# Performance work log

Hardware: AMD Instinct MI355X
Metric: run time of the kernel (lower is better)

## Reference

```python
import jax, jax.numpy as jnp
import numpy as np

EPS = 1e-6


def _att_vector(x, W, b, sharp2, th2, is_last):
    """AttentionVector on a 2D payoff slice.
    x: (N, a, m). W: (1, 2), b: (1,). Returns (N, a)."""
    # compare_param: pair (x[n,j,k], x[n,i,k]) -> Linear(2,1) -> sigmoid -> mean over k
    # Linear on the concat pair is w00*x[n,j,k] + w01*x[n,i,k] + b, so we fuse it.
    lin = W[0, 0] * x[:, None, :, :] + W[0, 1] * x[:, :, None, :] + b[0]  # (N,a,a,m)
    c = jnp.mean(jax.nn.sigmoid(lin), axis=3)  # (N,a,a)
    # max_normalize over dim 2
    c = c / (jnp.max(c, axis=2, keepdims=True) + EPS)
    # compute_player_mask
    m = jnp.mean(c, axis=2)  # (N,a)
    m = jax.nn.relu(m * sharp2[0] + th2[0])
    m = jax.nn.softmax(m, axis=1)
    if not is_last:
        m = m / (jnp.max(m, axis=1, keepdims=True) + EPS)
    return m


def setup_inputs() -> dict:
    key = jax.random.key(0)
    ks = jax.random.split(key, 16)
    N, a1, a2, f = 128, 64, 64, 2
    inp = {
        "x": jax.random.normal(ks[0], (N, f, a1, a2), dtype=jnp.float32),
        "fc_W": jax.random.normal(ks[1], (2, 2), dtype=jnp.float32) * 0.5,
        "fc_b": jax.random.normal(ks[2], (2,), dtype=jnp.float32) * 0.1,
        "p1_W": jax.random.normal(ks[3], (1, 2), dtype=jnp.float32) * 0.5,
        "p1_b": jax.random.normal(ks[4], (1,), dtype=jnp.float32) * 0.1,
        "p1_sharp": jnp.ones((1,), dtype=jnp.float32),
        "p1_th": jnp.zeros((1,), dtype=jnp.float32),
        "p2_W": jax.random.normal(ks[5], (1, 2), dtype=jnp.float32) * 0.5,
        "p2_b": jax.random.normal(ks[6], (1,), dtype=jnp.float32) * 0.1,
        "p2_sharp": jnp.ones((1,), dtype=jnp.float32),
        "p2_th": jnp.zeros((1,), dtype=jnp.float32),
        "out_W": jax.random.normal(ks[7], (1, 2), dtype=jnp.float32) * 0.5,
        "out_b": jax.random.normal(ks[8], (1,), dtype=jnp.float32) * 0.1,
        "out_sharp": jnp.ones((1,), dtype=jnp.float32),
        "out_th": jnp.zeros((1,), dtype=jnp.float32),
    }
    return inp


def reference(x, fc_W, fc_b, p1_W, p1_b, p1_sharp, p1_th,
              p2_W, p2_b, p2_sharp, p2_th,
              out_W, out_b, out_sharp, out_th):
    # x: (N, f=2, a1, a2) -> (N, a1, a2, f)
    h = jnp.transpose(x, (0, 2, 3, 1))
    # is_fc_first: Linear(2, 2) + ReLU on last dim
    h = jax.nn.relu(h @ fc_W.T + fc_b)  # (N,a1,a2,2)
    # one AttentionModule (module_layers=1, not simult)
    vec1 = _att_vector(h[..., 0], p1_W, p1_b, p1_sharp, p1_th, is_last=False)  # (N,a1)
    h = h * vec1[:, :, None, None]
    pl2 = jnp.transpose(h[..., 1], (0, 2, 1))  # (N,a2,a1)
    vec2 = _att_vector(pl2, p2_W, p2_b, p2_sharp, p2_th, is_last=False)  # (N,a2)
    h = h * vec2[:, None, :, None]
    # with_last: final AttentionVector (is_last=True) on player-1 channel
    out = _att_vector(h[..., 0], out_W, out_b, out_sharp, out_th, is_last=True)  # (N,a1)
    return out
```

## Files before the change

kernel.cpp:

```cpp
#include <hip/hip_runtime.h>


constexpr int A   = 64;
constexpr int PAD = 65;
constexpr float L2E  = 1.4426950408889634f;
constexpr float EPSF = 1e-6f;

__device__ __forceinline__ float bcast(float v, int srcLane) {
    return __int_as_float(__builtin_amdgcn_readlane(__float_as_int(v), srcLane));
}
__device__ __forceinline__ float rcpf(float v) { return __builtin_amdgcn_rcpf(v); }
__device__ __forceinline__ float ex2(float v)  { return __builtin_amdgcn_exp2f(v); }

__device__ __forceinline__ void att2q(const float* __restrict__ prow,
                                      const float* __restrict__ qL,
                                      int row0, int lane,
                                      float* __restrict__ mbuf,
                                      float* __restrict__ mg)
{
    const float qreg0 = qL[row0 * PAD + lane];
    const float qreg1 = qL[(row0 + 1) * PAD + lane];
    float acc0 = 0.f, acc1 = 0.f;
#pragma unroll 1
    for (int c = 0; c < 4; ++c) {
        float pk[16];
#pragma unroll
        for (int t = 0; t < 16; ++t) pk[t] = prow[c * 16 + t];
#pragma unroll
        for (int t = 0; t < 16; ++t) {
            const int k = c * 16 + t;
            float q0 = bcast(qreg0, k);
            float q1 = bcast(qreg1, k);
            acc0 += rcpf(fmaf(pk[t], q0, 1.0f));
            acc1 += rcpf(fmaf(pk[t], q1, 1.0f));
        }
    }
    float s0 = acc0, m0 = acc0, s1 = acc1, m1 = acc1;
#pragma unroll
    for (int off = 1; off < 64; off <<= 1) {
        s0 += __shfl_xor(s0, off, 64);
        m0 = fmaxf(m0, __shfl_xor(m0, off, 64));
        s1 += __shfl_xor(s1, off, 64);
        m1 = fmaxf(m1, __shfl_xor(m1, off, 64));
    }
    if (lane == 0) {
        float v0 = (s0 * (1.0f / 4096.0f)) / (m0 * (1.0f / 64.0f) + EPSF);
        float v1 = (s1 * (1.0f / 4096.0f)) / (m1 * (1.0f / 64.0f) + EPSF);
        mbuf[row0]     = v0;
        mbuf[row0 + 1] = v1;
        __hip_atomic_store(mg + row0,     v0 + 2.0f, __ATOMIC_RELAXED, __HIP_MEMORY_SCOPE_AGENT);
        __hip_atomic_store(mg + row0 + 1, v1 + 2.0f, __ATOMIC_RELAXED, __HIP_MEMORY_SCOPE_AGENT);
    }
}

__device__ __forceinline__ float softmax64(float m, float sharp, float th, bool last)
{
    float v = fmaxf(0.f, m * sharp + th);
    float mx = v;
#pragma unroll
    for (int off = 1; off < 64; off <<= 1) mx = fmaxf(mx, __shfl_xor(mx, off, 64));
    float e = __expf(v - mx);
    float s = e;
#pragma unroll
    for (int off = 1; off < 64; off <<= 1) s += __shfl_xor(s, off, 64);
    float r = e / s;
    if (!last) {
        float rm = r;
#pragma unroll
        for (int off = 1; off < 64; off <<= 1) rm = fmaxf(rm, __shfl_xor(rm, off, 64));
        r = r / (rm + EPSF);
    }
    return r;
}

__device__ __forceinline__ float exch_soft(const float* __restrict__ mbuf,
                                           const float* __restrict__ mg,
                                           int half, int lane,
                                           float sharp, float th, bool last)
{
    float mv;
    if ((lane >> 5) == half) {
        mv = mbuf[lane];
    } else {
        const float* p = mg + lane;
        for (;;) {
            float f = __hip_atomic_load(p, __ATOMIC_RELAXED, __HIP_MEMORY_SCOPE_AGENT);
            unsigned u = __float_as_uint(f);
            if ((u >> 23) == 0x80u) { mv = f - 2.0f; break; }
            __builtin_amdgcn_s_sleep(1);
        }
    }
    return softmax64(mv, sharp, th, last);
}

__global__ __launch_bounds__(1024, 2)
void attn_half(const float* __restrict__ x,
               const float* __restrict__ fcW, const float* __restrict__ fcb,
               const float* __restrict__ p1W, const float* __restrict__ p1b,
               const float* __restrict__ p1s, const float* __restrict__ p1t,
               const float* __restrict__ p2W, const float* __restrict__ p2b,
               const float* __restrict__ p2s, const float* __restrict__ p2t,
               const float* __restrict__ oW,  const float* __restrict__ ob,
               const float* __restrict__ os,  const float* __restrict__ ot,
               float* __restrict__ mglob,
               float* __restrict__ out)
{
    __shared__ float pL[A * PAD];
    __shared__ float qL[A * PAD];
    __shared__ float mbuf[A];
    __shared__ float v1buf[A], v2buf[A];

    const int tid = threadIdx.x, lane = tid & 63, wv = tid >> 6;
    const int n = blockIdx.x >> 1, half = blockIdx.x & 1;
    const int row0 = half * 32 + wv * 2;
    const int i = tid >> 4, j = (tid & 15) * 4;
    float* mg = mglob + (size_t)n * 3 * A;

    const float4* x0v = (const float4*)(x + (size_t)n * 2 * A * A);
    const float4* x1v = x0v + (A * A / 4);
    const float4 a = x0v[tid];
    const float4 c = x1v[tid];
    const float w00 = fcW[0], w01 = fcW[1], w10 = fcW[2], w11 = fcW[3];
    const float b0 = fcb[0], b1 = fcb[1];
    const float h0v[4] = { fmaxf(0.f, w00 * a.x + w01 * c.x + b0),
                           fmaxf(0.f, w00 * a.y + w01 * c.y + b0),
                           fmaxf(0.f, w00 * a.z + w01 * c.z + b0),
                           fmaxf(0.f, w00 * a.w + w01 * c.w + b0) };
    const float h1v[4] = { fmaxf(0.f, w10 * a.x + w11 * c.x + b1),
                           fmaxf(0.f, w10 * a.y + w11 * c.y + b1),
                           fmaxf(0.f, w10 * a.z + w11 * c.z + b1),
                           fmaxf(0.f, w10 * a.w + w11 * c.w + b1) };

    {
        const float W0 = p1W[0], W1 = p1W[1], bb = p1b[0];
#pragma unroll
        for (int t = 0; t < 4; ++t) {
            pL[i * PAD + j + t] = ex2(-L2E * (W0 * h0v[t] + bb));
            qL[i * PAD + j + t] = ex2(-L2E * (W1 * h0v[t]));
        }
    }
    __syncthreads();
    att2q(pL + lane * PAD, qL, row0, lane, mbuf, mg);
    __syncthreads();
    if (wv == 0) v1buf[lane] = exch_soft(mbuf, mg, half, lane, p1s[0], p1t[0], false);
    __syncthreads();

    {
        const float W0 = p2W[0], W1 = p2W[1], bb = p2b[0];
        const float sc = v1buf[i];
#pragma unroll
        for (int t = 0; t < 4; ++t) {
            float hv = h1v[t] * sc;
            pL[(j + t) * PAD + i] = ex2(-L2E * (W0 * hv + bb));
            qL[(j + t) * PAD + i] = ex2(-L2E * (W1 * hv));
        }
    }
    __syncthreads();
    att2q(pL + lane * PAD, qL, row0, lane, mbuf, mg + A);
    __syncthreads();
    if (wv == 0) v2buf[lane] = exch_soft(mbuf, mg + A, half, lane, p2s[0], p2t[0], false);
    __syncthreads();

    {
        const float W0 = oW[0], W1 = oW[1], bb = ob[0];
        const float sc = v1buf[i];
        const float4 v2q = *(const float4*)&v2buf[j];
        const float v2a[4] = { v2q.x, v2q.y, v2q.z, v2q.w };
#pragma unroll
        for (int t = 0; t < 4; ++t) {
            float hv = h0v[t] * sc * v2a[t];
            pL[i * PAD + j + t] = ex2(-L2E * (W0 * hv + bb));
            qL[i * PAD + j + t] = ex2(-L2E * (W1 * hv));
        }
    }
    __syncthreads();
    att2q(pL + lane * PAD, qL, row0, lane, mbuf, mg + 2 * A);
    __syncthreads();

    if (wv == 0) {
        float r = exch_soft(mbuf, mg + 2 * A, half, lane, os[0], ot[0], true);
        if ((lane >> 5) == half) out[(size_t)n * A + lane] = r;
    }
}

extern "C" void kernel_launch(void* const* d_in, const int* in_sizes, int n_in,
                              void* d_out, int out_size, void* d_ws, size_t ws_size,
                              hipStream_t stream)
{
    (void)n_in; (void)out_size; (void)ws_size;
    const float* x   = (const float*)d_in[0];
    const float* fcW = (const float*)d_in[1];
    const float* fcb = (const float*)d_in[2];
    const float* p1W = (const float*)d_in[3];
    const float* p1b = (const float*)d_in[4];
    const float* p1s = (const float*)d_in[5];
    const float* p1t = (const float*)d_in[6];
    const float* p2W = (const float*)d_in[7];
    const float* p2b = (const float*)d_in[8];
    const float* p2s = (const float*)d_in[9];
    const float* p2t = (const float*)d_in[10];
    const float* oW  = (const float*)d_in[11];
    const float* ob  = (const float*)d_in[12];
    const float* os  = (const float*)d_in[13];
    const float* ot  = (const float*)d_in[14];
    float* out = (float*)d_out;

    const int N = in_sizes[0] / (2 * A * A);
    float* mglob = (float*)d_ws;

    attn_half<<<2 * N, 1024, 0, stream>>>(x, fcW, fcb,
                                          p1W, p1b, p1s, p1t,
                                          p2W, p2b, p2s, p2t,
                                          oW, ob, os, ot, mglob, out);
}
```

Measured before the change: 105.5 us.

## Poll global flags for all rows, drop LDS staging barrier, remap block pairing

Wave 0 now reads all 64 row means from the global exchange buffer by polling, including its own half's. This removes the shared mbuf staging and the barrier that followed each att2q. Block pairing changes so the two halves of a sample are blocks n and n+128 instead of adjacent blocks, and only half 0 runs the final softmax and writes the output. This cuts block-level synchronisation and redundant final work. The cost is more atomic polling traffic, and a deadlock risk if the partner block (n+128) is not co-resident. The block index mapping also hardcodes N=128.

```diff
diff --git a/kernel.cpp b/kernel.cpp
--- a/kernel.cpp
+++ b/kernel.cpp
@@ -12,10 +12,18 @@
 __device__ __forceinline__ float rcpf(float v) { return __builtin_amdgcn_rcpf(v); }
 __device__ __forceinline__ float ex2(float v)  { return __builtin_amdgcn_exp2f(v); }
 
+__device__ __forceinline__ float poll_m(const float* __restrict__ p) {
+    for (;;) {
+        float f = __hip_atomic_load(p, __ATOMIC_RELAXED, __HIP_MEMORY_SCOPE_AGENT);
+        unsigned u = __float_as_uint(f);
+        if ((u >> 23) == 0x80u) return f - 2.0f;
+        __builtin_amdgcn_s_sleep(1);
+    }
+}
+
 __device__ __forceinline__ void att2q(const float* __restrict__ prow,
                                       const float* __restrict__ qL,
                                       int row0, int lane,
-                                      float* __restrict__ mbuf,
                                       float* __restrict__ mg)
 {
     const float qreg0 = qL[row0 * PAD + lane];
@@ -46,8 +54,6 @@
     if (lane == 0) {
         float v0 = (s0 * (1.0f / 4096.0f)) / (m0 * (1.0f / 64.0f) + EPSF);
         float v1 = (s1 * (1.0f / 4096.0f)) / (m1 * (1.0f / 64.0f) + EPSF);
-        mbuf[row0]     = v0;
-        mbuf[row0 + 1] = v1;
         __hip_atomic_store(mg + row0,     v0 + 2.0f, __ATOMIC_RELAXED, __HIP_MEMORY_SCOPE_AGENT);
         __hip_atomic_store(mg + row0 + 1, v1 + 2.0f, __ATOMIC_RELAXED, __HIP_MEMORY_SCOPE_AGENT);
     }
@@ -73,26 +79,6 @@
     return r;
 }
 
-__device__ __forceinline__ float exch_soft(const float* __restrict__ mbuf,
-                                           const float* __restrict__ mg,
-                                           int half, int lane,
-                                           float sharp, float th, bool last)
-{
-    float mv;
-    if ((lane >> 5) == half) {
-        mv = mbuf[lane];
-    } else {
-        const float* p = mg + lane;
-        for (;;) {
-            float f = __hip_atomic_load(p, __ATOMIC_RELAXED, __HIP_MEMORY_SCOPE_AGENT);
-            unsigned u = __float_as_uint(f);
-            if ((u >> 23) == 0x80u) { mv = f - 2.0f; break; }
-            __builtin_amdgcn_s_sleep(1);
-        }
-    }
-    return softmax64(mv, sharp, th, last);
-}
-
 __global__ __launch_bounds__(1024, 2)
 void attn_half(const float* __restrict__ x,
                const float* __restrict__ fcW, const float* __restrict__ fcb,
@@ -107,11 +93,10 @@
 {
     __shared__ float pL[A * PAD];
     __shared__ float qL[A * PAD];
-    __shared__ float mbuf[A];
     __shared__ float v1buf[A], v2buf[A];
 
     const int tid = threadIdx.x, lane = tid & 63, wv = tid >> 6;
-    const int n = blockIdx.x >> 1, half = blockIdx.x & 1;
+    const int n = blockIdx.x & 127, half = blockIdx.x >> 7;
     const int row0 = half * 32 + wv * 2;
     const int i = tid >> 4, j = (tid & 15) * 4;
     float* mg = mglob + (size_t)n * 3 * A;
@@ -140,9 +125,8 @@
         }
     }
     __syncthreads();
-    att2q(pL + lane * PAD, qL, row0, lane, mbuf, mg);
-    __syncthreads();
-    if (wv == 0) v1buf[lane] = exch_soft(mbuf, mg, half, lane, p1s[0], p1t[0], false);
+    att2q(pL + lane * PAD, qL, row0, lane, mg);
+    if (wv == 0) v1buf[lane] = softmax64(poll_m(mg + lane), p1s[0], p1t[0], false);
     __syncthreads();
 
     {
@@ -156,9 +140,8 @@
         }
     }
     __syncthreads();
-    att2q(pL + lane * PAD, qL, row0, lane, mbuf, mg + A);
-    __syncthreads();
-    if (wv == 0) v2buf[lane] = exch_soft(mbuf, mg + A, half, lane, p2s[0], p2t[0], false);
+    att2q(pL + lane * PAD, qL, row0, lane, mg + A);
+    if (wv == 0) v2buf[lane] = softmax64(poll_m(mg + A + lane), p2s[0], p2t[0], false);
     __syncthreads();
 
     {
@@ -174,12 +157,11 @@
         }
     }
     __syncthreads();
-    att2q(pL + lane * PAD, qL, row0, lane, mbuf, mg + 2 * A);
-    __syncthreads();
+    att2q(pL + lane * PAD, qL, row0, lane, mg + 2 * A);
 
-    if (wv == 0) {
-        float r = exch_soft(mbuf, mg + 2 * A, half, lane, os[0], ot[0], true);
-        if ((lane >> 5) == half) out[(size_t)n * A + lane] = r;
+    if (half == 0 && wv == 0) {
+        float r = softmax64(poll_m(mg + 2 * A + lane), os[0], ot[0], true);
+        out[(size_t)n * A + lane] = r;
     }
 }
 
```

Result: no change. 107.1 us (+1.5%).
